# Kernel optimization log

Measured on AMD Instinct MI355X. Metric: run time of the kernel, lower is better.

Reference implementation:

```python
import jax, jax.numpy as jnp
import numpy as np
from jax import lax

B, T, D, H = 4, 2048, 1024, 8
DK = D // H        # head qk dim (expand_k=1.0) = 128
DV = 2 * D // H    # head v dim (expand_v=2.0) = 256
C = 64             # retention chunk size


def setup_inputs() -> dict:
    key = jax.random.key(0)
    ks = jax.random.split(key, 7)
    s = 0.02
    return {
        "x": jax.random.normal(ks[0], (B, T, D), jnp.float32),
        "Wq": jax.random.normal(ks[1], (D, H * DK), jnp.float32) * s,
        "Wk": jax.random.normal(ks[2], (D, H * DK), jnp.float32) * s,
        "Wv": jax.random.normal(ks[3], (D, H * DV), jnp.float32) * s,
        "Wg": jax.random.normal(ks[4], (D, H * DV), jnp.float32) * s,
        "Wo": jax.random.normal(ks[5], (H * DV, D), jnp.float32) * s,
        "norm_w": jnp.ones((DV,), jnp.float32),
    }


def _rope(x):
    # x: [B,T,H,DK]; GPT-NeoX style (non-interleaved) rotary, base 10000
    half = DK // 2
    inv = 1.0 / (10000.0 ** (jnp.arange(0, DK, 2, dtype=jnp.float32) / DK))
    f = jnp.arange(T, dtype=jnp.float32)[:, None] * inv[None, :]  # [T, half]
    cos = jnp.cos(f)[None, :, None, :]
    sin = jnp.sin(f)[None, :, None, :]
    x1, x2 = x[..., :half], x[..., half:]
    return jnp.concatenate([x1 * cos - x2 * sin, x2 * cos + x1 * sin], axis=-1)


def _retention(q, k, v):
    # chunked decay-gated linear attention (RetNet retention)
    # q,k: [B,T,H,DK], v: [B,T,H,DV]; recurrence S_t = g*S_{t-1} + k_t^T v_t, o_t = q_t S_t
    N = T // C
    gamma = 1.0 - 2.0 ** (-5.0 - jnp.arange(H, dtype=jnp.float32))  # [H] per-head decay
    i = jnp.arange(C, dtype=jnp.float32)
    expo = i[:, None] - i[None, :]                                   # [C,C]
    M = jnp.where(expo >= 0, gamma[:, None, None] ** expo[None], 0.0)  # [H,C,C] intra-chunk decay mask
    dec_q = gamma[:, None] ** (i + 1.0)        # [H,C] decay of state seen by q_i
    dec_k = gamma[:, None] ** (C - 1.0 - i)    # [H,C] decay of k_j into end-of-chunk state
    gC = gamma ** C

    def to_chunks(t):
        return t.reshape(B, N, C, H, -1).transpose(1, 0, 3, 2, 4)  # [N,B,H,C,d]

    qs, kcs, vcs = to_chunks(q), to_chunks(k), to_chunks(v)

    def step(S, inp):
        qc, kc, vc = inp  # [B,H,C,DK],[B,H,C,DK],[B,H,C,DV]
        attn = jnp.einsum('bhid,bhjd->bhij', qc, kc) * M[None]
        o_intra = jnp.einsum('bhij,bhje->bhie', attn, vc)
        o_inter = jnp.einsum('bhid,bhde->bhie', qc, S) * dec_q[None, :, :, None]
        kv = jnp.einsum('bhjd,bhje->bhde', kc * dec_k[None, :, :, None], vc)
        S_new = gC[None, :, None, None] * S + kv
        return S_new, o_intra + o_inter

    S0 = jnp.zeros((B, H, DK, DV), q.dtype)
    _, os_ = lax.scan(step, S0, (qs, kcs, vcs))  # os_: [N,B,H,C,DV]
    return os_.transpose(1, 0, 3, 2, 4).reshape(B, T, H, DV)


def reference(x, Wq, Wk, Wv, Wg, Wo, norm_w):
    q = (x @ Wq).reshape(B, T, H, DK)
    k = (x @ Wk).reshape(B, T, H, DK)
    v = (x @ Wv).reshape(B, T, H, DV)
    g = (x @ Wg).reshape(B, T, H, DV)
    q, k = _rope(q), _rope(k)
    q = q * (DK ** -0.5)
    o = _retention(q, k, v)
    # fused per-head RMSNorm + swish output gate (FusedRMSNormSwishGate)
    rms = jnp.sqrt(jnp.mean(o * o, axis=-1, keepdims=True) + 1e-5)
    o = (o / rms) * norm_w
    o = o * g * jax.nn.sigmoid(g)
    return o.reshape(B, T, H * DV) @ Wo
```

## Files before the change

### kernel.cpp

```cpp
#include <hip/hip_runtime.h>
#include <hip/hip_bf16.h>
#include <cstdint>
#include <cstddef>

using f32x4 = __attribute__((ext_vector_type(4))) float;
using s16x8 = __attribute__((ext_vector_type(8))) short;
using s16x4 = __attribute__((ext_vector_type(4))) short;

#define DEVINL __device__ __forceinline__

static constexpr int T_LEN  = 2048;
static constexpr int MROWS  = 8192;
static constexpr int NCHUNK = 32;

DEVINL float bf2f(short s){
  unsigned u = ((unsigned)(unsigned short)s) << 16;
  return __builtin_bit_cast(float, u);
}
DEVINL short f2bf(float f){
  unsigned u = __builtin_bit_cast(unsigned, f);
  u = (u + 0x7fffu + ((u >> 16) & 1u)) >> 16;
  return (short)(unsigned short)u;
}

#define GLOAD16(gp, lp) \
  __builtin_amdgcn_global_load_lds((__attribute__((address_space(1))) void*)(gp), \
                                   (__attribute__((address_space(3))) void*)(lp), 16, 0, 0)

#define MFMA16(a, b, c) __builtin_amdgcn_mfma_f32_16x16x32_bf16((a), (b), (c), 0, 0, 0)

__global__ __launch_bounds__(256) void cvt_f32_bf16(const float* __restrict__ in,
                                                    short* __restrict__ out, int n4){
  int i = blockIdx.x * 256 + threadIdx.x;
  if (i >= n4) return;
  float4 v = ((const float4*)in)[i];
  short4 o;
  o.x = f2bf(v.x); o.y = f2bf(v.y); o.z = f2bf(v.z); o.w = f2bf(v.w);
  ((short4*)out)[i] = o;
}

__global__ __launch_bounds__(256) void tr_w(const float* __restrict__ in,
                                            short* __restrict__ out, int R, int C){
  __shared__ float tile[32][33];
  int c0 = blockIdx.x * 32, r0 = blockIdx.y * 32;
  int tx = threadIdx.x, ty = threadIdx.y;
  #pragma unroll
  for (int i = 0; i < 4; ++i){
    int r = ty + i * 8;
    tile[r][tx] = in[(size_t)(r0 + r) * C + c0 + tx];
  }
  __syncthreads();
  #pragma unroll
  for (int i = 0; i < 4; ++i){
    int c = ty + i * 8;
    out[(size_t)(c0 + c) * R + r0 + tx] = f2bf(tile[tx][c]);
  }
}

__global__ __launch_bounds__(256) void tr_k_decay(const short* __restrict__ in,
                                                  short* __restrict__ out){
  __shared__ float tile[32][33];
  int c0 = blockIdx.x * 32, r0 = blockIdx.y * 32;
  int tx = threadIdx.x, ty = threadIdx.y;
  #pragma unroll
  for (int i = 0; i < 4; ++i){
    int r = ty + i * 8;
    tile[r][tx] = bf2f(in[(size_t)(r0 + r) * 1024 + c0 + tx]);
  }
  __syncthreads();
  #pragma unroll
  for (int i = 0; i < 4; ++i){
    int c  = c0 + ty + i * 8;
    int h  = c >> 7;
    float lg = log2f(1.0f - exp2f(-(float)(5 + h)));
    int srow = r0 + tx;
    int j = srow & 63;
    float dec = exp2f((float)(63 - j) * lg);
    out[(size_t)c * MROWS + srow] = f2bf(tile[tx][ty + i * 8] * dec);
  }
}

__global__ __launch_bounds__(256) void rope_table(float* __restrict__ tab){
  int i = blockIdx.x * 256 + threadIdx.x;
  int t = i >> 6, d = i & 63;
  float inv = exp2f(-(float)d * (13.287712379549449f / 64.0f));
  float f = (float)t * inv;
  float s, c;
  sincosf(f, &s, &c);
  tab[2 * i]     = c;
  tab[2 * i + 1] = s;
}

__global__ __launch_bounds__(256) void rope_inplace(short* __restrict__ qk,
                                                    const float* __restrict__ tab,
                                                    float scale, int bake){
  int idx = blockIdx.x * 256 + threadIdx.x;
  int bt  = idx >> 9, rem = idx & 511;
  int h   = rem >> 6, d = rem & 63;
  int t   = bt & (T_LEN - 1);
  float2 cs = ((const float2*)tab)[t * 64 + d];
  float mult = scale;
  if (bake){
    float lg = log2f(1.0f - exp2f(-(float)(5 + h)));
    mult *= exp2f((float)((t & 63) + 1) * lg);
  }
  size_t base = (size_t)bt * 1024 + h * 128 + d;
  float x1 = bf2f(qk[base]), x2 = bf2f(qk[base + 64]);
  qk[base]      = f2bf((x1 * cs.x - x2 * cs.y) * mult);
  qk[base + 64] = f2bf((x2 * cs.x + x1 * cs.y) * mult);
}

DEVINL s16x8 frag64(const short* buf, int row, int ks, int lhi){
  int ch = (ks * 4 + lhi) ^ (row & 7);
  return *(const s16x8*)&buf[row * 64 + ch * 8];
}

template<int MODE>
__global__ __launch_bounds__(512, 2) void gemm256(const short* __restrict__ A,
                                                  const short* __restrict__ Bt,
                                                  void* __restrict__ o0, void* __restrict__ o1,
                                                  void* __restrict__ o2, void* __restrict__ o3,
                                                  int K, int nt, int NT){
  constexpr int BM   = (MODE == 2 ? 128 : 256);
  constexpr int ABUF = BM * 64;
  constexpr int MF   = BM / 32;
  constexpr int RPP  = MF / 4;
  __shared__ alignas(16) short LBUF[3 * ABUF + 2 * 16384];
  short* const BB = LBUF + 3 * ABUF;
  const int tid = threadIdx.x, wave = tid >> 6, lane = tid & 63;
  const int l15 = lane & 15, lhi = lane >> 4;
  const int wm = (wave >> 2) * (BM / 2), wn = (wave & 3) * 64;
  const int MG  = (gridDim.x >> 3) / NT;
  const int xcd = blockIdx.x & 7, idx = blockIdx.x >> 3;
  const int mi  = idx % MG, nn = idx / MG;
  const int m0  = (xcd * MG + mi) * BM, n0 = nn * 256;
  const short* Ag = A + (size_t)m0 * K;
  const short* Bg = Bt + (size_t)n0 * K;
  const int sr = lane >> 3;
  const int gc = ((lane & 7) ^ sr) * 8;
  f32x4 acc[MF][4] = {};

  auto stageA = [&](int t, int half){
    short* lb = LBUF + (t % 3) * ABUF;
    size_t k0 = (size_t)t * 64;
    if constexpr (BM == 256){
      #pragma unroll
      for (int c = 0; c < 2; ++c){
        int r0 = half * 128 + c * 64;
        GLOAD16(Ag + (size_t)(r0 + wave * 8 + sr) * K + k0 + gc, lb + (r0 + wave * 8) * 64);
      }
    } else {
      int r0 = half * 64;
      GLOAD16(Ag + (size_t)(r0 + wave * 8 + sr) * K + k0 + gc, lb + (r0 + wave * 8) * 64);
    }
  };
  auto stageB = [&](int t, int half){
    short* lb = BB + (t & 1) * 16384;
    size_t k0 = (size_t)t * 64;
    #pragma unroll
    for (int c = 0; c < 2; ++c){
      int r0 = half * 128 + c * 64;
      GLOAD16(Bg + (size_t)(r0 + wave * 8 + sr) * K + k0 + gc, lb + (r0 + wave * 8) * 64);
    }
  };

  stageA(0, 0); stageA(0, 1); stageB(0, 0); stageB(0, 1);
  stageA(1, 0); stageA(1, 1); stageB(1, 0); stageB(1, 1);
  if constexpr (BM == 256) asm volatile("s_waitcnt vmcnt(8)" ::: "memory");
  else                     asm volatile("s_waitcnt vmcnt(6)" ::: "memory");
  __builtin_amdgcn_sched_barrier(0);
  __builtin_amdgcn_s_barrier();

  for (int t = 0; t < nt; ++t){
    const short* Ab = LBUF + (t % 3) * ABUF;
    const short* Bb = BB + (t & 1) * 16384;
    s16x8 bfr[2][4];
    #pragma unroll
    for (int q = 0; q < 4; ++q){
      if (q == 0){
        #pragma unroll
        for (int ks = 0; ks < 2; ++ks)
          #pragma unroll
          for (int nf = 0; nf < 4; ++nf)
            bfr[ks][nf] = frag64(Bb, wn + nf * 16 + l15, ks, lhi);
      }
      s16x8 af[RPP][2];
      #pragma unroll
      for (int i = 0; i < RPP; ++i)
        #pragma unroll
        for (int ks = 0; ks < 2; ++ks)
          af[i][ks] = frag64(Ab, wm + (RPP * q + i) * 16 + l15, ks, lhi);
      if (t + 2 < nt){
        if (q == 0) stageA(t + 2, 0);
        if (q == 1) stageA(t + 2, 1);
        if (q == 2) stageB(t + 2, 0);
        if (q == 3) stageB(t + 2, 1);
      }
      __builtin_amdgcn_sched_barrier(0);
      __builtin_amdgcn_s_barrier();
      asm volatile("s_waitcnt lgkmcnt(0)" ::: "memory");
      __builtin_amdgcn_sched_barrier(0);
      __builtin_amdgcn_s_setprio(1);
      #pragma unroll
      for (int i = 0; i < RPP; ++i)
        #pragma unroll
        for (int nf = 0; nf < 4; ++nf)
          #pragma unroll
          for (int ks = 0; ks < 2; ++ks)
            acc[RPP * q + i][nf] = MFMA16(af[i][ks], bfr[ks][nf], acc[RPP * q + i][nf]);
      __builtin_amdgcn_s_setprio(0);
      if (q == 3){
        if (t < nt - 2){
          if constexpr (BM == 256) asm volatile("s_waitcnt vmcnt(8)" ::: "memory");
          else                     asm volatile("s_waitcnt vmcnt(6)" ::: "memory");
        } else if (t == nt - 2){
          asm volatile("s_waitcnt vmcnt(0)" ::: "memory");
        }
        __builtin_amdgcn_sched_barrier(0);
      }
      __builtin_amdgcn_s_barrier();
    }
  }
  if (MODE == 2){
    float* dst = (float*)o0;
    #pragma unroll
    for (int mf = 0; mf < MF; ++mf){
      int rb = m0 + wm + mf * 16 + 4 * lhi;
      #pragma unroll
      for (int nf = 0; nf < 4; ++nf){
        int col = n0 + wn + nf * 16 + l15;
        #pragma unroll
        for (int r = 0; r < 4; ++r) dst[(size_t)(rb + r) * 1024 + col] = acc[mf][nf][r];
      }
    }
  } else {
    if (n0 < 2048){
      short* dst = (short*)(n0 < 1024 ? o0 : o1);
      int cb = (n0 & 1023) + wn;
      #pragma unroll
      for (int mf = 0; mf < MF; ++mf){
        int rb = m0 + wm + mf * 16 + 4 * lhi;
        #pragma unroll
        for (int nf = 0; nf < 4; ++nf){
          int col = cb + nf * 16 + l15;
          #pragma unroll
          for (int r = 0; r < 4; ++r) dst[(size_t)(rb + r) * 1024 + col] = f2bf(acc[mf][nf][r]);
        }
      }
    } else if (n0 < 4096){
      short* dst = (short*)o2;
      #pragma unroll
      for (int mf = 0; mf < MF; ++mf){
        int rb = m0 + wm + mf * 16 + 4 * lhi;
        #pragma unroll
        for (int nf = 0; nf < 4; ++nf){
          int e = (n0 - 2048) + wn + nf * 16 + l15;
          s16x4 pk;
          #pragma unroll
          for (int r = 0; r < 4; ++r) pk[r] = f2bf(acc[mf][nf][r]);
          *(s16x4*)&dst[(size_t)e * MROWS + rb] = pk;
        }
      }
    } else {
      short* dst = (short*)o3;
      int cb = (n0 - 4096) + wn;
      #pragma unroll
      for (int mf = 0; mf < MF; ++mf){
        int rb = m0 + wm + mf * 16 + 4 * lhi;
        #pragma unroll
        for (int nf = 0; nf < 4; ++nf){
          int col = cb + nf * 16 + l15;
          #pragma unroll
          for (int r = 0; r < 4; ++r) dst[(size_t)(rb + r) * 2048 + col] = f2bf(acc[mf][nf][r]);
        }
      }
    }
  }
}

__global__ __launch_bounds__(256) void ret_scan(const short* __restrict__ kT,
                                                const short* __restrict__ vT,
                                                short* __restrict__ ST){
  __shared__ alignas(16) short kbuf[3][4096];
  __shared__ alignas(16) short vbuf[3][4096];
  const int tid = threadIdx.x, wave = tid >> 6, lane = tid & 63;
  const int db = blockIdx.x & 1, eb = blockIdx.x >> 1;
  const int h = blockIdx.y, b = blockIdx.z;
  const int d0 = db * 64, e0 = eb * 64;
  const float lg = log2f(1.0f - exp2f(-(float)(5 + h)));
  const float gC = exp2f(64.0f * lg);
  f32x4 Sacc[4] = {};
  const int srow = wave * 8 + (lane >> 3);
  const int sc   = lane & 7;

  auto STAGE = [&](int n, int buf){
    size_t rowbase = (size_t)(b * T_LEN + n * 64);
    #pragma unroll
    for (int c = 0; c < 2; ++c){
      int r = c * 32 + srow;
      int gc = sc ^ (r & 7);
      GLOAD16(kT + (size_t)(h * 128 + d0 + r) * MROWS + rowbase + gc * 8,
              &kbuf[buf][c * 2048 + wave * 512]);
    }
    #pragma unroll
    for (int c = 0; c < 2; ++c){
      int r = c * 32 + srow;
      int gc = sc ^ (r & 7);
      GLOAD16(vT + (size_t)(h * 256 + e0 + r) * MROWS + rowbase + gc * 8,
              &vbuf[buf][c * 2048 + wave * 512]);
    }
  };

  STAGE(0, 0);
  STAGE(1, 1);
  for (int n = 0; n < NCHUNK; ++n){
    const int buf = n % 3;
    if (n + 2 < NCHUNK) STAGE(n + 2, (n + 2) % 3);
    if (n > 0){
      size_t stb = (((size_t)n * 4 + b) * 8 + h) * 32768;
      int dbase = d0 + 16 * wave + 4 * (lane >> 4);
      #pragma unroll
      for (int nf = 0; nf < 4; ++nf){
        int e = e0 + nf * 16 + (lane & 15);
        s16x4 pk;
        #pragma unroll
        for (int r = 0; r < 4; ++r) pk[r] = f2bf(Sacc[nf][r]);
        *(s16x4*)&ST[stb + (size_t)e * 128 + dbase] = pk;
      }
    }
    if (n == 0)       asm volatile("s_waitcnt vmcnt(8)"  ::: "memory");
    else if (n < 30)  asm volatile("s_waitcnt vmcnt(12)" ::: "memory");
    else if (n == 30) asm volatile("s_waitcnt vmcnt(8)"  ::: "memory");
    else              asm volatile("s_waitcnt vmcnt(4)"  ::: "memory");
    __builtin_amdgcn_s_barrier();
    __builtin_amdgcn_sched_barrier(0);
    #pragma unroll
    for (int nf = 0; nf < 4; ++nf)
      #pragma unroll
      for (int r = 0; r < 4; ++r) Sacc[nf][r] *= gC;
    #pragma unroll
    for (int ks = 0; ks < 2; ++ks){
      int d = 16 * wave + (lane & 15);
      int chA = (ks * 4 + (lane >> 4)) ^ (d & 7);
      s16x8 af = *(const s16x8*)&kbuf[buf][d * 64 + chA * 8];
      #pragma unroll
      for (int nf = 0; nf < 4; ++nf){
        int e = nf * 16 + (lane & 15);
        int chB = (ks * 4 + (lane >> 4)) ^ (e & 7);
        s16x8 bv = *(const s16x8*)&vbuf[buf][e * 64 + chB * 8];
        Sacc[nf] = MFMA16(af, bv, Sacc[nf]);
      }
    }
    __builtin_amdgcn_s_barrier();
    __builtin_amdgcn_sched_barrier(0);
  }
}

__global__ __launch_bounds__(256, 2) void ret_fused(const short* __restrict__ q,
                                                    const short* __restrict__ k,
                                                    const short* __restrict__ vT,
                                                    const short* __restrict__ ST,
                                                    const short* __restrict__ g,
                                                    const float* __restrict__ nw,
                                                    short* __restrict__ y){
  __shared__ alignas(16) short GS[16384];
  __shared__ alignas(16) float SS[256];
  __shared__ alignas(16) short XS[16896];
  short* PS = XS;
  short* YT = XS;
  const int tid = threadIdx.x, wave = tid >> 6, lane = tid & 63;
  const int l15 = lane & 15, lhi = lane >> 4;
  const int n = blockIdx.x, h = blockIdx.y, b = blockIdx.z;
  const size_t rowbase = (size_t)(b * T_LEN + n * 64);
  {
    int row = wave * 2 + (lane >> 5), sc32 = lane & 31;
    #pragma unroll
    for (int c = 0; c < 8; ++c){
      int r = c * 8 + row;
      GLOAD16(g + (rowbase + r) * 2048 + h * 256 + sc32 * 8, &GS[c * 2048 + wave * 512]);
    }
  }
  s16x8 Qf[4][4];
  #pragma unroll
  for (int rf = 0; rf < 4; ++rf)
    #pragma unroll
    for (int ks = 0; ks < 4; ++ks)
      Qf[rf][ks] = *(const s16x8*)&q[(rowbase + rf * 16 + l15) * 1024 + h * 128 + ks * 32 + lhi * 8];
  s16x8 Kf[4];
  #pragma unroll
  for (int ks = 0; ks < 4; ++ks)
    Kf[ks] = *(const s16x8*)&k[(rowbase + wave * 16 + l15) * 1024 + h * 128 + ks * 32 + lhi * 8];
  f32x4 accP[4] = {};
  #pragma unroll
  for (int ks = 0; ks < 4; ++ks)
    #pragma unroll
    for (int nf = 0; nf < 4; ++nf)
      accP[nf] = MFMA16(Kf[ks], Qf[nf][ks], accP[nf]);
  const float lg = log2f(1.0f - exp2f(-(float)(5 + h)));
  {
    int jb = wave * 16 + 4 * lhi;
    float dj[4];
    #pragma unroll
    for (int r = 0; r < 4; ++r) dj[r] = exp2f(-(float)(jb + r + 1) * lg);
    #pragma unroll
    for (int nf = 0; nf < 4; ++nf){
      int i = nf * 16 + l15;
      s16x4 pk;
      #pragma unroll
      for (int r = 0; r < 4; ++r)
        pk[r] = f2bf((i >= jb + r) ? accP[nf][r] * dj[r] : 0.0f);
      *(s16x4*)&PS[i * 72 + jb] = pk;
    }
  }
  f32x4 acc[4][4] = {};
  if (n){
    size_t stb = (((size_t)n * 4 + b) * 8 + h) * 32768;
    #pragma unroll
    for (int ks = 0; ks < 4; ++ks){
      s16x8 Sf[4];
      #pragma unroll
      for (int nf = 0; nf < 4; ++nf){
        int e = wave * 64 + nf * 16 + l15;
        Sf[nf] = *(const s16x8*)&ST[stb + (size_t)e * 128 + ks * 32 + lhi * 8];
      }
      #pragma unroll
      for (int mf = 0; mf < 4; ++mf)
        #pragma unroll
        for (int nf = 0; nf < 4; ++nf)
          acc[mf][nf] = MFMA16(Qf[mf][ks], Sf[nf], acc[mf][nf]);
    }
  }
  s16x8 Vf[2][4];
  #pragma unroll
  for (int ks2 = 0; ks2 < 2; ++ks2)
    #pragma unroll
    for (int nf = 0; nf < 4; ++nf){
      int e = wave * 64 + nf * 16 + l15;
      Vf[ks2][nf] = *(const s16x8*)&vT[(size_t)(h * 256 + e) * MROWS + rowbase + ks2 * 32 + lhi * 8];
    }
  __syncthreads();
  #pragma unroll
  for (int ks2 = 0; ks2 < 2; ++ks2){
    s16x8 Pf[4];
    #pragma unroll
    for (int mf = 0; mf < 4; ++mf)
      Pf[mf] = *(const s16x8*)&PS[(mf * 16 + l15) * 72 + ks2 * 32 + lhi * 8];
    #pragma unroll
    for (int mf = 0; mf < 4; ++mf)
      #pragma unroll
      for (int nf = 0; nf < 4; ++nf)
        acc[mf][nf] = MFMA16(Pf[mf], Vf[ks2][nf], acc[mf][nf]);
  }
  float ssp[4][4];
  #pragma unroll
  for (int mf = 0; mf < 4; ++mf)
    #pragma unroll
    for (int r = 0; r < 4; ++r){
      float s = 0.f;
      #pragma unroll
      for (int nf = 0; nf < 4; ++nf) s += acc[mf][nf][r] * acc[mf][nf][r];
      #pragma unroll
      for (int off = 8; off >= 1; off >>= 1) s += __shfl_xor(s, off, 64);
      ssp[mf][r] = s;
    }
  if (l15 == 0){
    #pragma unroll
    for (int mf = 0; mf < 4; ++mf)
      #pragma unroll
      for (int r = 0; r < 4; ++r){
        int row = mf * 16 + 4 * lhi + r;
        SS[row * 4 + wave] = ssp[mf][r];
      }
  }
  __syncthreads();
  #pragma unroll
  for (int mf = 0; mf < 4; ++mf){
    float rr[4];
    #pragma unroll
    for (int r = 0; r < 4; ++r){
      int row = mf * 16 + 4 * lhi + r;
      f32x4 s4 = *(const f32x4*)&SS[row * 4];
      float tot = s4[0] + s4[1] + s4[2] + s4[3];
      rr[r] = __builtin_amdgcn_rsqf(tot * (1.0f / 256.0f) + 1e-5f);
    }
    #pragma unroll
    for (int nf = 0; nf < 4; ++nf){
      int e = wave * 64 + nf * 16 + l15;
      float nwe = nw[e];
      #pragma unroll
      for (int r = 0; r < 4; ++r){
        int row = mf * 16 + 4 * lhi + r;
        float gf = bf2f(GS[row * 256 + e]);
        float sig = __builtin_amdgcn_rcpf(1.0f + exp2f(gf * -1.4426950408889634f));
        YT[row * 264 + e] = f2bf(acc[mf][nf][r] * rr[r] * nwe * gf * sig);
      }
    }
  }
  __syncthreads();
  #pragma unroll
  for (int it = 0; it < 8; ++it){
    int flat = it * 2048 + tid * 8;
    int row = flat >> 8, e = flat & 255;
    s16x8 v = *(const s16x8*)&YT[row * 264 + e];
    *(s16x8*)&y[(rowbase + row) * 2048 + h * 256 + e] = v;
  }
}

extern "C" void kernel_launch(void* const* d_in, const int* in_sizes, int n_in,
                              void* d_out, int out_size, void* d_ws, size_t ws_size,
                              hipStream_t stream){
  const float* x  = (const float*)d_in[0];
  const float* Wq = (const float*)d_in[1];
  const float* Wk = (const float*)d_in[2];
  const float* Wv = (const float*)d_in[3];
  const float* Wg = (const float*)d_in[4];
  const float* Wo = (const float*)d_in[5];
  const float* nw = (const float*)d_in[6];
  float* out = (float*)d_out;

  char* w = (char*)d_ws;
  short* xb  = (short*)w;               w += (size_t)8192 * 1024 * 2;
  short* WT  = (short*)w;               w += (size_t)6144 * 1024 * 2;
  short* kTt = (short*)w;               w += (size_t)1024 * 8192 * 2;
  short* qb  = (short*)w;               w += (size_t)8192 * 1024 * 2;
  short* kb  = (short*)w;               w += (size_t)8192 * 1024 * 2;
  short* vT  = (short*)w;               w += (size_t)2048 * 8192 * 2;
  short* gb  = (short*)w;               w += (size_t)8192 * 2048 * 2;
  short* STb = (short*)w;               w += (size_t)32 * 4 * 8 * 32768 * 2;
  short* WoT = (short*)w;               w += (size_t)1024 * 2048 * 2;
  short* yb  = (short*)d_ws;
  float* tab = (float*)STb;

  cvt_f32_bf16<<<8192, 256, 0, stream>>>(x, xb, 8192 * 1024 / 4);
  dim3 tb(32, 8);
  tr_w<<<dim3(32, 32), tb, 0, stream>>>(Wq, WT,                       1024, 1024);
  tr_w<<<dim3(32, 32), tb, 0, stream>>>(Wk, WT + (size_t)1024 * 1024, 1024, 1024);
  tr_w<<<dim3(64, 32), tb, 0, stream>>>(Wv, WT + (size_t)2048 * 1024, 1024, 2048);
  tr_w<<<dim3(64, 32), tb, 0, stream>>>(Wg, WT + (size_t)4096 * 1024, 1024, 2048);
  tr_w<<<dim3(32, 64), tb, 0, stream>>>(Wo, WoT,                      2048, 1024);
  rope_table<<<512, 256, 0, stream>>>(tab);

  gemm256<3><<<768, 512, 0, stream>>>(xb, WT, qb, kb, vT, gb, 1024, 16, 24);

  rope_inplace<<<16384, 256, 0, stream>>>(qb, tab, 0.08838834764831845f, 1);
  rope_inplace<<<16384, 256, 0, stream>>>(kb, tab, 1.0f, 0);
  tr_k_decay<<<dim3(32, 256), tb, 0, stream>>>(kb, kTt);

  ret_scan <<<dim3(8, 8, 4),  256, 0, stream>>>(kTt, vT, STb);
  ret_fused<<<dim3(32, 8, 4), 256, 0, stream>>>(qb, kb, vT, STb, gb, nw, yb);

  gemm256<2><<<256, 512, 0, stream>>>(yb, WoT, out, nullptr, nullptr, nullptr, 2048, 32, 4);
}
```

Baseline: 288.3 us.

## Prefetch next A fragments from LDS in GEMM loop and vectorize epilogue stores

The GEMM main loop now double-buffers A-fragment register reads, loading the next quarter's fragments (and the next tile's first quarter) while the current MFMAs run. It also replaces the full lgkmcnt(0) waits with partial waits and moves the vmcnt wait to mid-tile. For outputs that are not transposed, the MFMA operands are swapped so each lane holds contiguous columns, which allows vectorized float4/short4 row stores in the epilogue. The risks are higher register pressure from the extra fragment buffers and subtle synchronization hazards on the triple-buffered LDS.

```diff
diff --git a/kernel.cpp b/kernel.cpp
--- a/kernel.cpp
+++ b/kernel.cpp
@@ -28,6 +28,9 @@
                                    (__attribute__((address_space(3))) void*)(lp), 16, 0, 0)
 
 #define MFMA16(a, b, c) __builtin_amdgcn_mfma_f32_16x16x32_bf16((a), (b), (c), 0, 0, 0)
+#define SBAR()  __builtin_amdgcn_sched_barrier(0)
+#define WAITLGKM(n) asm volatile("s_waitcnt lgkmcnt(" #n ")" ::: "memory")
+#define WAITVM(n)   asm volatile("s_waitcnt vmcnt(" #n ")" ::: "memory")
 
 __global__ __launch_bounds__(256) void cvt_f32_bf16(const float* __restrict__ in,
                                                     short* __restrict__ out, int n4){
@@ -138,6 +141,7 @@
   const short* Bg = Bt + (size_t)n0 * K;
   const int sr = lane >> 3;
   const int gc = ((lane & 7) ^ sr) * 8;
+  const bool vreg = (MODE == 3) && (n0 >= 2048 && n0 < 4096);
   f32x4 acc[MF][4] = {};
 
   auto stageA = [&](int t, int half){
@@ -164,115 +168,122 @@
     }
   };
 
+  s16x8 bfr[2][4];
+  s16x8 afA[RPP][2], afB[RPP][2];
+  auto readAf = [&](s16x8 (&dst)[RPP][2], const short* Ab, int q){
+    #pragma unroll
+    for (int i = 0; i < RPP; ++i)
+      #pragma unroll
+      for (int ks = 0; ks < 2; ++ks)
+        dst[i][ks] = frag64(Ab, wm + (RPP * q + i) * 16 + l15, ks, lhi);
+  };
+  auto readB = [&](const short* Bb){
+    #pragma unroll
+    for (int ks = 0; ks < 2; ++ks)
+      #pragma unroll
+      for (int nf = 0; nf < 4; ++nf)
+        bfr[ks][nf] = frag64(Bb, wn + nf * 16 + l15, ks, lhi);
+  };
+
   stageA(0, 0); stageA(0, 1); stageB(0, 0); stageB(0, 1);
   stageA(1, 0); stageA(1, 1); stageB(1, 0); stageB(1, 1);
-  if constexpr (BM == 256) asm volatile("s_waitcnt vmcnt(8)" ::: "memory");
-  else                     asm volatile("s_waitcnt vmcnt(6)" ::: "memory");
-  __builtin_amdgcn_sched_barrier(0);
+  if constexpr (BM == 256) WAITVM(8); else WAITVM(6);
+  SBAR();
   __builtin_amdgcn_s_barrier();
+  readAf(afA, LBUF, 0);
 
   for (int t = 0; t < nt; ++t){
-    const short* Ab = LBUF + (t % 3) * ABUF;
-    const short* Bb = BB + (t & 1) * 16384;
-    s16x8 bfr[2][4];
+    const short* Ab  = LBUF + (t % 3) * ABUF;
+    const short* Anx = LBUF + ((t + 1) % 3) * ABUF;
+    const short* Bb  = BB + (t & 1) * 16384;
     #pragma unroll
     for (int q = 0; q < 4; ++q){
-      if (q == 0){
-        #pragma unroll
-        for (int ks = 0; ks < 2; ++ks)
-          #pragma unroll
-          for (int nf = 0; nf < 4; ++nf)
-            bfr[ks][nf] = frag64(Bb, wn + nf * 16 + l15, ks, lhi);
-      }
-      s16x8 af[RPP][2];
-      #pragma unroll
-      for (int i = 0; i < RPP; ++i)
-        #pragma unroll
-        for (int ks = 0; ks < 2; ++ks)
-          af[i][ks] = frag64(Ab, wm + (RPP * q + i) * 16 + l15, ks, lhi);
+      __builtin_amdgcn_s_barrier();
+      if (q == 2){
+        if (t + 2 < nt){ if constexpr (BM == 256) WAITVM(4); else WAITVM(2); }
+        else           { WAITVM(0); }
+        SBAR();
+      }
       if (t + 2 < nt){
         if (q == 0) stageA(t + 2, 0);
         if (q == 1) stageA(t + 2, 1);
         if (q == 2) stageB(t + 2, 0);
         if (q == 3) stageB(t + 2, 1);
       }
-      __builtin_amdgcn_sched_barrier(0);
-      __builtin_amdgcn_s_barrier();
-      asm volatile("s_waitcnt lgkmcnt(0)" ::: "memory");
-      __builtin_amdgcn_sched_barrier(0);
+      bool tail = (q == 3) && (t + 1 >= nt);
+      if (q == 0){ readB(Bb); SBAR(); readAf(afB, Ab, 1); }
+      else if (q == 1){ readAf(afA, Ab, 2); }
+      else if (q == 2){ readAf(afB, Ab, 3); }
+      else if (!tail) { readAf(afA, Anx, 0); }
+      if (tail){ WAITLGKM(0); }
+      else if constexpr (RPP == 2){ WAITLGKM(4); }
+      else                        { WAITLGKM(2); }
+      SBAR();
       __builtin_amdgcn_s_setprio(1);
-      #pragma unroll
-      for (int i = 0; i < RPP; ++i)
+      if (vreg){
         #pragma unroll
-        for (int nf = 0; nf < 4; ++nf)
+        for (int i = 0; i < RPP; ++i)
           #pragma unroll
-          for (int ks = 0; ks < 2; ++ks)
-            acc[RPP * q + i][nf] = MFMA16(af[i][ks], bfr[ks][nf], acc[RPP * q + i][nf]);
+          for (int nf = 0; nf < 4; ++nf)
+            #pragma unroll
+            for (int ks = 0; ks < 2; ++ks)
+              acc[RPP * q + i][nf] = (q & 1)
+                ? MFMA16(afB[i][ks], bfr[ks][nf], acc[RPP * q + i][nf])
+                : MFMA16(afA[i][ks], bfr[ks][nf], acc[RPP * q + i][nf]);
+      } else {
+        #pragma unroll
+        for (int i = 0; i < RPP; ++i)
+          #pragma unroll
+          for (int nf = 0; nf < 4; ++nf)
+            #pragma unroll
+            for (int ks = 0; ks < 2; ++ks)
+              acc[RPP * q + i][nf] = (q & 1)
+                ? MFMA16(bfr[ks][nf], afB[i][ks], acc[RPP * q + i][nf])
+                : MFMA16(bfr[ks][nf], afA[i][ks], acc[RPP * q + i][nf]);
+      }
       __builtin_amdgcn_s_setprio(0);
-      if (q == 3){
-        if (t < nt - 2){
-          if constexpr (BM == 256) asm volatile("s_waitcnt vmcnt(8)" ::: "memory");
-          else                     asm volatile("s_waitcnt vmcnt(6)" ::: "memory");
-        } else if (t == nt - 2){
-          asm volatile("s_waitcnt vmcnt(0)" ::: "memory");
-        }
-        __builtin_amdgcn_sched_barrier(0);
-      }
-      __builtin_amdgcn_s_barrier();
     }
   }
   if (MODE == 2){
     float* dst = (float*)o0;
     #pragma unroll
     for (int mf = 0; mf < MF; ++mf){
+      int m = m0 + wm + mf * 16 + l15;
+      #pragma unroll
+      for (int nf = 0; nf < 4; ++nf){
+        int nb = n0 + wn + nf * 16 + 4 * lhi;
+        *(float4*)&dst[(size_t)m * 1024 + nb] = *(float4*)&acc[mf][nf];
+      }
+    }
+  } else if (vreg){
+    short* dst = (short*)o2;
+    #pragma unroll
+    for (int mf = 0; mf < MF; ++mf){
       int rb = m0 + wm + mf * 16 + 4 * lhi;
       #pragma unroll
       for (int nf = 0; nf < 4; ++nf){
-        int col = n0 + wn + nf * 16 + l15;
+        int e = (n0 - 2048) + wn + nf * 16 + l15;
+        s16x4 pk;
         #pragma unroll
-        for (int r = 0; r < 4; ++r) dst[(size_t)(rb + r) * 1024 + col] = acc[mf][nf][r];
+        for (int r = 0; r < 4; ++r) pk[r] = f2bf(acc[mf][nf][r]);
+        *(s16x4*)&dst[(size_t)e * MROWS + rb] = pk;
       }
     }
   } else {
-    if (n0 < 2048){
-      short* dst = (short*)(n0 < 1024 ? o0 : o1);
-      int cb = (n0 & 1023) + wn;
-      #pragma unroll
-      for (int mf = 0; mf < MF; ++mf){
-        int rb = m0 + wm + mf * 16 + 4 * lhi;
+    short* dst; int ld, cb;
+    if (n0 < 1024)      { dst = (short*)o0; ld = 1024; cb = n0; }
+    else if (n0 < 2048) { dst = (short*)o1; ld = 1024; cb = n0 - 1024; }
+    else                { dst = (short*)o3; ld = 2048; cb = n0 - 4096; }
+    #pragma unroll
+    for (int mf = 0; mf < MF; ++mf){
+      int m = m0 + wm + mf * 16 + l15;
+      #pragma unroll
+      for (int nf = 0; nf < 4; ++nf){
+        int nb = cb + wn + nf * 16 + 4 * lhi;
+        s16x4 pk;
         #pragma unroll
-        for (int nf = 0; nf < 4; ++nf){
-          int col = cb + nf * 16 + l15;
-          #pragma unroll
-          for (int r = 0; r < 4; ++r) dst[(size_t)(rb + r) * 1024 + col] = f2bf(acc[mf][nf][r]);
-        }
-      }
-    } else if (n0 < 4096){
-      short* dst = (short*)o2;
-      #pragma unroll
-      for (int mf = 0; mf < MF; ++mf){
-        int rb = m0 + wm + mf * 16 + 4 * lhi;
-        #pragma unroll
-        for (int nf = 0; nf < 4; ++nf){
-          int e = (n0 - 2048) + wn + nf * 16 + l15;
-          s16x4 pk;
-          #pragma unroll
-          for (int r = 0; r < 4; ++r) pk[r] = f2bf(acc[mf][nf][r]);
-          *(s16x4*)&dst[(size_t)e * MROWS + rb] = pk;
-        }
-      }
-    } else {
-      short* dst = (short*)o3;
-      int cb = (n0 - 4096) + wn;
-      #pragma unroll
-      for (int mf = 0; mf < MF; ++mf){
-        int rb = m0 + wm + mf * 16 + 4 * lhi;
-        #pragma unroll
-        for (int nf = 0; nf < 4; ++nf){
-          int col = cb + nf * 16 + l15;
-          #pragma unroll
-          for (int r = 0; r < 4; ++r) dst[(size_t)(rb + r) * 2048 + col] = f2bf(acc[mf][nf][r]);
-        }
+        for (int r = 0; r < 4; ++r) pk[r] = f2bf(acc[mf][nf][r]);
+        *(s16x4*)&dst[(size_t)m * ld + nb] = pk;
       }
     }
   }
@@ -298,15 +309,15 @@
     #pragma unroll
     for (int c = 0; c < 2; ++c){
       int r = c * 32 + srow;
-      int gc = sc ^ (r & 7);
-      GLOAD16(kT + (size_t)(h * 128 + d0 + r) * MROWS + rowbase + gc * 8,
+      int gc2 = sc ^ (r & 7);
+      GLOAD16(kT + (size_t)(h * 128 + d0 + r) * MROWS + rowbase + gc2 * 8,
               &kbuf[buf][c * 2048 + wave * 512]);
     }
     #pragma unroll
     for (int c = 0; c < 2; ++c){
       int r = c * 32 + srow;
-      int gc = sc ^ (r & 7);
-      GLOAD16(vT + (size_t)(h * 256 + e0 + r) * MROWS + rowbase + gc * 8,
+      int gc2 = sc ^ (r & 7);
+      GLOAD16(vT + (size_t)(h * 256 + e0 + r) * MROWS + rowbase + gc2 * 8,
               &vbuf[buf][c * 2048 + wave * 512]);
     }
   };
@@ -328,12 +339,12 @@
         *(s16x4*)&ST[stb + (size_t)e * 128 + dbase] = pk;
       }
     }
-    if (n == 0)       asm volatile("s_waitcnt vmcnt(8)"  ::: "memory");
-    else if (n < 30)  asm volatile("s_waitcnt vmcnt(12)" ::: "memory");
-    else if (n == 30) asm volatile("s_waitcnt vmcnt(8)"  ::: "memory");
-    else              asm volatile("s_waitcnt vmcnt(4)"  ::: "memory");
+    if (n == 0)       WAITVM(8);
+    else if (n < 30)  WAITVM(12);
+    else if (n == 30) WAITVM(8);
+    else              WAITVM(4);
     __builtin_amdgcn_s_barrier();
-    __builtin_amdgcn_sched_barrier(0);
+    SBAR();
     #pragma unroll
     for (int nf = 0; nf < 4; ++nf)
       #pragma unroll
@@ -352,7 +363,7 @@
       }
     }
     __builtin_amdgcn_s_barrier();
-    __builtin_amdgcn_sched_barrier(0);
+    SBAR();
   }
 }
 
```

New measurement: 311.4 us. 1.08x slower.
